# Performance work log

Hardware: AMD Instinct MI355X
Metric: run time of the kernel (lower is better)

## Reference

```python
import jax, jax.numpy as jnp
import numpy as np
from jax import lax

K = 16
EPS = 1e-5


def setup_inputs() -> dict:
    key = jax.random.key(0)
    k1, k2, k3 = jax.random.split(key, 3)
    x = jax.random.normal(k1, (8, 4096, 64), jnp.float32)
    pos = jax.random.normal(k2, (8, 4096, 3), jnp.float32)
    # nn.Linear(64,128), xavier_uniform weight, zero bias
    limit = float(np.sqrt(6.0 / (64 + 128)))
    W = jax.random.uniform(k3, (128, 64), jnp.float32, -limit, limit)
    b = jnp.zeros((128,), jnp.float32)
    gamma = jnp.ones((128,), jnp.float32)   # BN weight
    beta = jnp.zeros((128,), jnp.float32)   # BN bias
    return {"x": x, "pos": pos, "W": W, "b": b, "gamma": gamma, "beta": beta,
            "n_sampling": 1024}


def _fps(pos3, n_sampling):
    """Farthest point sampling starting at index 0. pos3: [bz,N,3] -> [bz,S] int32."""
    bz, N, _ = pos3.shape

    def step(carry, _):
        min_d, last = carry                                   # [bz,N], [bz]
        lastp = jnp.take_along_axis(pos3, last[:, None, None], axis=1)  # [bz,1,3]
        d = jnp.sum((pos3 - lastp) ** 2, axis=-1)             # [bz,N]
        min_d = jnp.minimum(min_d, d)
        nxt = jnp.argmax(min_d, axis=1).astype(jnp.int32)
        return (min_d, nxt), last

    init = (jnp.full((bz, N), 1e10, pos3.dtype), jnp.zeros((bz,), jnp.int32))
    _, idx = lax.scan(step, init, None, length=n_sampling)    # [S,bz]
    return idx.T                                              # [bz,S]


def _knn_idx(pos3, fps_idx, k):
    """k nearest neighbors (by squared L2) of sampled points among all N points."""
    spos = jnp.take_along_axis(pos3, fps_idx[..., None], axis=1)        # [bz,S,3]
    # ||a-b||^2 = |a|^2 + |b|^2 - 2 a.b, avoids [bz,S,N,3] intermediate
    d = (jnp.sum(spos ** 2, -1)[:, :, None]
         + jnp.sum(pos3 ** 2, -1)[:, None, :]
         - 2.0 * jnp.einsum('bsd,bnd->bsn', spos, pos3))               # [bz,S,N]
    _, idx = lax.top_k(-d, k)                                           # [bz,S,k]
    return idx


def reference(x, pos, W, b, gamma, beta, n_sampling):
    pos3 = pos[..., :3]
    fps_idx = _fps(pos3, n_sampling)                          # [bz,S]
    knn_idx = _knn_idx(pos3, fps_idx, K)                      # [bz,S,K]

    # Linear -> BatchNorm1d (training-mode batch stats, biased var) -> ReLU
    h = jnp.einsum('bnf,of->bno', x, W) + b                   # [bz,N,128]
    mean = h.mean(axis=(0, 1))
    var = h.var(axis=(0, 1))
    h = (h - mean) / jnp.sqrt(var + EPS) * gamma + beta
    h = jax.nn.relu(h)

    # gather k-NN features and max-pool (same math as expand+repeat+gather+max)
    gathered = jax.vmap(lambda hb, ib: hb[ib])(h, knn_idx)    # [bz,S,K,128]
    sampled_knn_x = gathered.max(axis=2)                      # [bz,S,128]

    sampled_pos = jnp.take_along_axis(pos, fps_idx[..., None], axis=1)  # [bz,S,3]
    return sampled_knn_x, sampled_pos
```

## Files before the change

### kernel.cpp

```cpp
#include <hip/hip_runtime.h>
#include <stdint.h>

typedef unsigned long long ull;
typedef float f32x2 __attribute__((ext_vector_type(2)));

#define NBATCH 8
#define NPTS   4096
#define NS     1024
#define NK     16
#define NF     64
#define NO     128

#define FT  256
#define PPT 16

static __device__ __forceinline__ ull umax64(ull a, ull b) { return a > b ? a : b; }
static __device__ __forceinline__ ull umin64(ull a, ull b) { return a < b ? a : b; }

static __device__ __forceinline__ float dist2(const float* plds, int i, float sx,
                                              float sy, float sz) {
  const float dx = plds[i * 3 + 0] - sx;
  const float dy = plds[i * 3 + 1] - sy;
  const float dz = plds[i * 3 + 2] - sz;
  return fmaf(dz, dz, fmaf(dy, dy, dx * dx));
}

static __device__ __forceinline__ ull dpp_min_u64(ull v) {
#define STEP(ctrl)                                                            \
  {                                                                           \
    const unsigned lo = (unsigned)v;                                          \
    const unsigned hi = (unsigned)(v >> 32);                                  \
    const unsigned olo = (unsigned)__builtin_amdgcn_update_dpp(               \
        (int)lo, (int)lo, ctrl, 0xf, 0xf, false);                             \
    const unsigned ohi = (unsigned)__builtin_amdgcn_update_dpp(               \
        (int)hi, (int)hi, ctrl, 0xf, 0xf, false);                             \
    const ull o = ((ull)ohi << 32) | olo;                                     \
    v = o < v ? o : v;                                                        \
  }
  STEP(0x111)
  STEP(0x112)
  STEP(0x114)
  STEP(0x118)
  STEP(0x142)
  STEP(0x143)
#undef STEP
  return v;
}

__global__ __launch_bounds__(256) void fps_stats_kernel(
    const float* __restrict__ pos, const float* __restrict__ x,
    const float* __restrict__ W, const float* __restrict__ bias,
    int* __restrict__ fps_idx, float* __restrict__ out_pos,
    float* __restrict__ partial) {
#pragma clang fp contract(off)
  const int t = threadIdx.x;
  __shared__ float plds[NPTS * 3];
  __shared__ __align__(16) ull wslot[2][4];
  __shared__ int widx_lds[NS];

  if (blockIdx.x >= 8) {
    const int blk = blockIdx.x - 8;
    const int c = t & 127;
    const int h = t >> 7;
    float* xl = plds;

    const float4* Wv = (const float4*)(W + c * NF);
    float4 w[16];
#pragma unroll
    for (int q = 0; q < 16; ++q) w[q] = Wv[q];
    const float bb = bias[c];

    const float4* src = (const float4*)(x + (size_t)blk * 128 * NF);
    float4* dst = (float4*)xl;
    for (int i = t; i < 128 * NF / 4; i += 256) dst[i] = src[i];
    __syncthreads();

    float s = 0.f, s2 = 0.f;
    for (int r = h * 64; r < h * 64 + 64; ++r) {
      const float4* xr = (const float4*)(xl + r * NF);
      float hh = bb;
#pragma unroll
      for (int q = 0; q < 16; ++q) {
        const float4 xv = xr[q];
        hh = fmaf(xv.x, w[q].x, hh);
        hh = fmaf(xv.y, w[q].y, hh);
        hh = fmaf(xv.z, w[q].z, hh);
        hh = fmaf(xv.w, w[q].w, hh);
      }
      s += hh;
      s2 = fmaf(hh, hh, s2);
    }
    partial[(blk * 2 + h) * 256 + c] = s;
    partial[(blk * 2 + h) * 256 + 128 + c] = s2;
    return;
  }

  const int b = blockIdx.x;
  const float* p = pos + (size_t)b * NPTS * 3;
  {
    const float4* src = (const float4*)p;
    float4* dst = (float4*)plds;
    for (int i = t; i < NPTS * 3 / 4; i += FT) dst[i] = src[i];
  }
  if (t == 0) widx_lds[0] = 0;
  __syncthreads();

  f32x2 px2[PPT / 2], py2[PPT / 2], pz2[PPT / 2], md2[PPT / 2];
#pragma unroll
  for (int jp = 0; jp < PPT / 2; ++jp) {
    const int i0 = t + FT * (2 * jp);
    const int i1 = i0 + FT;
    px2[jp] = (f32x2){plds[3 * i0 + 0], plds[3 * i1 + 0]};
    py2[jp] = (f32x2){plds[3 * i0 + 1], plds[3 * i1 + 1]};
    pz2[jp] = (f32x2){plds[3 * i0 + 2], plds[3 * i1 + 2]};
    md2[jp] = (f32x2){1e10f, 1e10f};
  }

  float lx = plds[0], ly = plds[1], lz = plds[2];

  for (int s = 1; s < NS; ++s) {
    const f32x2 lxv = (f32x2){lx, lx};
    const f32x2 lyv = (f32x2){ly, ly};
    const f32x2 lzv = (f32x2){lz, lz};
    f32x2 acc = (f32x2){0.f, 0.f};
#pragma unroll
    for (int jp = 0; jp < PPT / 2; ++jp) {
      const f32x2 dx = px2[jp] - lxv;
      const f32x2 dy = py2[jp] - lyv;
      const f32x2 dz = pz2[jp] - lzv;
      const f32x2 xx = dx * dx;
      const f32x2 yy = dy * dy;
      const f32x2 zz = dz * dz;
      const f32x2 sxy = xx + yy;
      const f32x2 d = sxy + zz;
      md2[jp] = __builtin_elementwise_min(md2[jp], d);
      acc = __builtin_elementwise_max(acc, md2[jp]);
    }
    float best = fmaxf(acc.x, acc.y);
    int lidx = 0;
#pragma unroll
    for (int jp = 0; jp < PPT / 2; ++jp) {
      if (md2[jp].x == best) lidx = t + FT * (2 * jp);
      if (md2[jp].y == best) lidx = t + FT * (2 * jp) + FT;
    }
#define CARRY_STEP(ctrl)                                                     \
    {                                                                        \
      const float bo = __int_as_float(__builtin_amdgcn_update_dpp(           \
          0, __float_as_int(best), ctrl, 0xf, 0xf, true));                   \
      const int io =                                                         \
          __builtin_amdgcn_update_dpp(0, lidx, ctrl, 0xf, 0xf, true);        \
      if (bo > best) {                                                       \
        best = bo;                                                           \
        lidx = io;                                                           \
      }                                                                      \
    }
    CARRY_STEP(0x111)
    CARRY_STEP(0x112)
    CARRY_STEP(0x114)
    CARRY_STEP(0x118)
    CARRY_STEP(0x142)
    CARRY_STEP(0x143)
#undef CARRY_STEP
    if ((t & 63) == 63)
      wslot[s & 1][t >> 6] = ((ull)__float_as_uint(best) << 32) | (unsigned)lidx;
    __syncthreads();
    const ull* wk = wslot[s & 1];
    const ull kk = umax64(umax64(wk[0], wk[1]), umax64(wk[2], wk[3]));
    const int widx = (int)(kk & 0xFFFFFFFFu);
    lx = plds[3 * widx + 0];
    ly = plds[3 * widx + 1];
    lz = plds[3 * widx + 2];
    if (t == 0) widx_lds[s] = widx;
  }

  __syncthreads();
  for (int i = t; i < NS; i += FT) {
    const int wi = widx_lds[i];
    fps_idx[b * NS + i] = wi;
    out_pos[((size_t)b * NS + i) * 3 + 0] = plds[3 * wi + 0];
    out_pos[((size_t)b * NS + i) * 3 + 1] = plds[3 * wi + 1];
    out_pos[((size_t)b * NS + i) * 3 + 2] = plds[3 * wi + 2];
  }
}

__global__ __launch_bounds__(1024) void stats_reduce_kernel(
    const float* __restrict__ partial, const float* __restrict__ gamma,
    const float* __restrict__ beta, float* __restrict__ ab) {
  const int t = threadIdx.x;
  const int c = t & 127;
  const int q = t >> 7;
  __shared__ double sred[1024], s2red[1024];
  double s = 0.0, s2 = 0.0;
#pragma unroll 4
  for (int r = q * 64; r < q * 64 + 64; ++r) {
    s += (double)partial[r * 256 + c];
    s2 += (double)partial[r * 256 + 128 + c];
  }
  sred[t] = s;
  s2red[t] = s2;
  __syncthreads();
  if (t < 128) {
    s = 0.0;
    s2 = 0.0;
#pragma unroll
    for (int qq = 0; qq < 8; ++qq) {
      s += sred[qq * 128 + t];
      s2 += s2red[qq * 128 + t];
    }
    const double n = 32768.0;
    const double mean = s / n;
    const double var = s2 / n - mean * mean;
    const float inv = (float)(1.0 / sqrt(var + 1e-5));
    const float scale = gamma[t] * inv;
    const float shift = beta[t] - (float)mean * scale;
    ab[t] = scale;
    ab[128 + t] = shift;
  }
}

__global__ __launch_bounds__(256) void knn_kernel(const float* __restrict__ pos,
                                                  const int* __restrict__ fps_idx,
                                                  int* __restrict__ knn_idx) {
  __shared__ float plds[NPTS * 3];
  const int b = blockIdx.y;
  const int t = threadIdx.x;
  const int s0 = blockIdx.x * 16;

  {
    const float4* src = (const float4*)(pos + (size_t)b * NPTS * 3);
    float4* dst = (float4*)plds;
    for (int i = t; i < NPTS * 3 / 4; i += 256) dst[i] = src[i];
  }
  __syncthreads();

  const int samp = t >> 4;
  const int chunk = t & 15;
  const int sidx = fps_idx[b * NS + s0 + samp];
  const float sx = plds[sidx * 3 + 0];
  const float sy = plds[sidx * 3 + 1];
  const float sz = plds[sidx * 3 + 2];

  ull k16[16];
#pragma unroll
  for (int k = 0; k < 16; ++k) k16[k] = 0xFFFFFFFF00000000ull | (unsigned)k;
  ull worst = 0xFFFFFFFF0000000Full;
  for (int j = 0; j < 256; ++j) {
    const int i = j * 16 + chunk;
    const float d = dist2(plds, i, sx, sy, sz);
    const ull key = ((ull)__float_as_uint(d) << 32) | (unsigned)i;
    if (key < worst) {
#pragma unroll
      for (int k = 0; k < 16; ++k) k16[k] = (k16[k] == worst) ? key : k16[k];
      ull w01 = umax64(k16[0], k16[1]);
      ull w2 = umax64(umax64(k16[2], k16[3]), umax64(k16[4], k16[5]));
      ull w3 = umax64(umax64(k16[6], k16[7]), umax64(k16[8], k16[9]));
      ull w4 = umax64(umax64(k16[10], k16[11]), umax64(k16[12], k16[13]));
      ull w5 = umax64(k16[14], k16[15]);
      worst = umax64(umax64(w01, w2), umax64(w3, umax64(w4, w5)));
    }
  }
  __syncthreads();
  ull* kbuf = (ull*)plds;
  {
    ull* dst = kbuf + samp * 256 + chunk * 16;
#pragma unroll
    for (int k = 0; k < 16; ++k) dst[k] = k16[k];
  }
  __syncthreads();

  const int wave = t >> 6;
  const int lane = t & 63;
  for (int si = 0; si < 4; ++si) {
    const int s = wave * 4 + si;
    const ull* src = kbuf + s * 256 + lane * 4;
    ull a0 = src[0], a1 = src[1], a2 = src[2], a3 = src[3];
    int kwin = 0;
#pragma unroll
    for (int k = 0; k < 16; ++k) {
      const ull mv = umin64(umin64(a0, a1), umin64(a2, a3));
      const ull wmin = dpp_min_u64(mv);
      const ull win = __shfl(wmin, 63, 64);
      if (lane == k) kwin = (int)(win & 0xFFFFFFFFu);
      a0 = (a0 == win) ? ~0ull : a0;
      a1 = (a1 == win) ? ~0ull : a1;
      a2 = (a2 == win) ? ~0ull : a2;
      a3 = (a3 == win) ? ~0ull : a3;
    }
    if (lane < 16)
      knn_idx[((size_t)b * NS + s0 + s) * NK + lane] = kwin;
  }
}

__global__ __launch_bounds__(256) void gather_kernel(
    const float* __restrict__ x, const float* __restrict__ W,
    const float* __restrict__ bias, const float* __restrict__ ab,
    const int* __restrict__ knn_idx, float* __restrict__ out) {
  __shared__ float xtile[64 * NF];
  const int b = blockIdx.y;
  const int t = threadIdx.x;
  const int s0 = blockIdx.x * 16;
  const int c2 = t & 63;
  const int g = t >> 6;

  float4 w0[16], w1[16];
  {
    const float4* Wv0 = (const float4*)(W + c2 * NF);
    const float4* Wv1 = (const float4*)(W + (c2 + 64) * NF);
#pragma unroll
    for (int q = 0; q < 16; ++q) {
      w0[q] = Wv0[q];
      w1[q] = Wv1[q];
    }
  }
  const float bb0 = bias[c2], bb1 = bias[c2 + 64];
  const float scale0 = ab[c2], scale1 = ab[c2 + 64];
  const float shift0 = ab[128 + c2], shift1 = ab[128 + c2 + 64];
  const float* xb = x + (size_t)b * NPTS * NF;

  for (int pass = 0; pass < 4; ++pass) {
    {
      const int r = t & 63;
      const int q0 = (t >> 6) * 4;
      const int idx =
          knn_idx[((size_t)b * NS + s0 + pass * 4 + (r >> 4)) * NK + (r & 15)];
      const float4* srow = (const float4*)(xb + (size_t)idx * NF);
      float4* drow = (float4*)(xtile + r * NF);
#pragma unroll
      for (int q = q0; q < q0 + 4; ++q) drow[q] = srow[q];
    }
    __syncthreads();

    float m0 = 0.0f, m1 = 0.0f;
#pragma unroll
    for (int k = 0; k < NK; ++k) {
      const float4* xr = (const float4*)(xtile + (g * 16 + k) * NF);
      float h0 = bb0, h1 = bb1;
#pragma unroll
      for (int q = 0; q < 16; ++q) {
        const float4 xv = xr[q];
        h0 = fmaf(xv.x, w0[q].x, h0);
        h0 = fmaf(xv.y, w0[q].y, h0);
        h0 = fmaf(xv.z, w0[q].z, h0);
        h0 = fmaf(xv.w, w0[q].w, h0);
        h1 = fmaf(xv.x, w1[q].x, h1);
        h1 = fmaf(xv.y, w1[q].y, h1);
        h1 = fmaf(xv.z, w1[q].z, h1);
        h1 = fmaf(xv.w, w1[q].w, h1);
      }
      h0 = fmaf(h0, scale0, shift0);
      h1 = fmaf(h1, scale1, shift1);
      h0 = h0 > 0.f ? h0 : 0.f;
      h1 = h1 > 0.f ? h1 : 0.f;
      m0 = m0 > h0 ? m0 : h0;
      m1 = m1 > h1 ? m1 : h1;
    }
    float* o = out + ((size_t)b * NS + s0 + pass * 4 + g) * NO;
    o[c2] = m0;
    o[c2 + 64] = m1;
    __syncthreads();
  }
}

extern "C" void kernel_launch(void* const* d_in, const int* in_sizes, int n_in,
                              void* d_out, int out_size, void* d_ws, size_t ws_size,
                              hipStream_t stream) {
  const float* x     = (const float*)d_in[0];
  const float* pos   = (const float*)d_in[1];
  const float* W     = (const float*)d_in[2];
  const float* bias  = (const float*)d_in[3];
  const float* gamma = (const float*)d_in[4];
  const float* beta  = (const float*)d_in[5];

  float* out_knn = (float*)d_out;
  float* out_pos = out_knn + (size_t)NBATCH * NS * NO;

  char* ws = (char*)d_ws;
  int* fps_idx   = (int*)(ws);
  float* partial = (float*)(ws + (32 << 10));
  int* knn_idx   = (int*)partial;
  float* ab      = (float*)(ws + (544 << 10));

  fps_stats_kernel<<<8 + 256, 256, 0, stream>>>(pos, x, W, bias, fps_idx,
                                                out_pos, partial);
  stats_reduce_kernel<<<1, 1024, 0, stream>>>(partial, gamma, beta, ab);
  knn_kernel<<<dim3(64, NBATCH), 256, 0, stream>>>(pos, fps_idx, knn_idx);
  gather_kernel<<<dim3(64, NBATCH), 256, 0, stream>>>(x, W, bias, ab, knn_idx,
                                                      out_knn);
}
```

Baseline: 910.3 us.

## Pack two FPS batches per 512-thread block sharing one barrier

Farthest-point sampling now runs two batch elements per workgroup of 512 threads, each half using its own LDS copy of positions and its own winner slots. Both halves pass the same per-iteration __syncthreads. Stats blocks are widened to 512 threads with an in-LDS pairwise reduction so the partial layout stays the same. This halves the number of FPS blocks and couples two independent serial chains at each barrier, which may add sync latency. The gain depends on how FPS blocks were placed across CUs before.

New measurement: 1.162 ms. 1.28x slower.

```diff
diff --git a/kernel.cpp b/kernel.cpp
--- a/kernel.cpp
+++ b/kernel.cpp
@@ -11,7 +11,6 @@
 #define NF     64
 #define NO     128
 
-#define FT  256
 #define PPT 16
 
 static __device__ __forceinline__ ull umax64(ull a, ull b) { return a > b ? a : b; }
@@ -47,22 +46,24 @@
   return v;
 }
 
-__global__ __launch_bounds__(256) void fps_stats_kernel(
+__global__ __launch_bounds__(512, 1) void fps_stats_kernel(
     const float* __restrict__ pos, const float* __restrict__ x,
     const float* __restrict__ W, const float* __restrict__ bias,
     int* __restrict__ fps_idx, float* __restrict__ out_pos,
     float* __restrict__ partial) {
 #pragma clang fp contract(off)
   const int t = threadIdx.x;
-  __shared__ float plds[NPTS * 3];
-  __shared__ __align__(16) ull wslot[2][4];
-  __shared__ int widx_lds[NS];
-
-  if (blockIdx.x >= 8) {
-    const int blk = blockIdx.x - 8;
+  __shared__ float plds[2][NPTS * 3];
+  __shared__ __align__(16) ull wslot[2][2][4];
+  __shared__ int widx_lds[2][NS];
+
+  if (blockIdx.x >= 4) {
+    const int blk = blockIdx.x - 4;
     const int c = t & 127;
     const int h = t >> 7;
-    float* xl = plds;
+    float* xl = plds[0];
+    float* sred = plds[1];
+    float* s2red = plds[1] + 512;
 
     const float4* Wv = (const float4*)(W + c * NF);
     float4 w[16];
@@ -72,11 +73,11 @@
 
     const float4* src = (const float4*)(x + (size_t)blk * 128 * NF);
     float4* dst = (float4*)xl;
-    for (int i = t; i < 128 * NF / 4; i += 256) dst[i] = src[i];
+    for (int i = t; i < 128 * NF / 4; i += 512) dst[i] = src[i];
     __syncthreads();
 
     float s = 0.f, s2 = 0.f;
-    for (int r = h * 64; r < h * 64 + 64; ++r) {
+    for (int r = h * 32; r < h * 32 + 32; ++r) {
       const float4* xr = (const float4*)(xl + r * NF);
       float hh = bb;
 #pragma unroll
@@ -90,33 +91,43 @@
       s += hh;
       s2 = fmaf(hh, hh, s2);
     }
-    partial[(blk * 2 + h) * 256 + c] = s;
-    partial[(blk * 2 + h) * 256 + 128 + c] = s2;
+    sred[t] = s;
+    s2red[t] = s2;
+    __syncthreads();
+    if (h < 2) {
+      s += sred[t + 256];
+      s2 += s2red[t + 256];
+      partial[(blk * 2 + h) * 256 + c] = s;
+      partial[(blk * 2 + h) * 256 + 128 + c] = s2;
+    }
     return;
   }
 
-  const int b = blockIdx.x;
-  const float* p = pos + (size_t)b * NPTS * 3;
+  const int grp = t >> 8;
+  const int tl = t & 255;
+  const int b = blockIdx.x * 2 + grp;
+  float* P = plds[grp];
+
   {
-    const float4* src = (const float4*)p;
-    float4* dst = (float4*)plds;
-    for (int i = t; i < NPTS * 3 / 4; i += FT) dst[i] = src[i];
-  }
-  if (t == 0) widx_lds[0] = 0;
+    const float4* src = (const float4*)(pos + (size_t)b * NPTS * 3);
+    float4* dst = (float4*)P;
+    for (int i = tl; i < NPTS * 3 / 4; i += 256) dst[i] = src[i];
+  }
+  if (tl == 0) widx_lds[grp][0] = 0;
   __syncthreads();
 
   f32x2 px2[PPT / 2], py2[PPT / 2], pz2[PPT / 2], md2[PPT / 2];
 #pragma unroll
   for (int jp = 0; jp < PPT / 2; ++jp) {
-    const int i0 = t + FT * (2 * jp);
-    const int i1 = i0 + FT;
-    px2[jp] = (f32x2){plds[3 * i0 + 0], plds[3 * i1 + 0]};
-    py2[jp] = (f32x2){plds[3 * i0 + 1], plds[3 * i1 + 1]};
-    pz2[jp] = (f32x2){plds[3 * i0 + 2], plds[3 * i1 + 2]};
+    const int i0 = tl + 256 * (2 * jp);
+    const int i1 = i0 + 256;
+    px2[jp] = (f32x2){P[3 * i0 + 0], P[3 * i1 + 0]};
+    py2[jp] = (f32x2){P[3 * i0 + 1], P[3 * i1 + 1]};
+    pz2[jp] = (f32x2){P[3 * i0 + 2], P[3 * i1 + 2]};
     md2[jp] = (f32x2){1e10f, 1e10f};
   }
 
-  float lx = plds[0], ly = plds[1], lz = plds[2];
+  float lx = P[0], ly = P[1], lz = P[2];
 
   for (int s = 1; s < NS; ++s) {
     const f32x2 lxv = (f32x2){lx, lx};
@@ -140,8 +151,8 @@
     int lidx = 0;
 #pragma unroll
     for (int jp = 0; jp < PPT / 2; ++jp) {
-      if (md2[jp].x == best) lidx = t + FT * (2 * jp);
-      if (md2[jp].y == best) lidx = t + FT * (2 * jp) + FT;
+      if (md2[jp].x == best) lidx = tl + 256 * (2 * jp);
+      if (md2[jp].y == best) lidx = tl + 256 * (2 * jp) + 256;
     }
 #define CARRY_STEP(ctrl)                                                     \
     {                                                                        \
@@ -161,25 +172,26 @@
     CARRY_STEP(0x142)
     CARRY_STEP(0x143)
 #undef CARRY_STEP
-    if ((t & 63) == 63)
-      wslot[s & 1][t >> 6] = ((ull)__float_as_uint(best) << 32) | (unsigned)lidx;
+    if ((tl & 63) == 63)
+      wslot[grp][s & 1][tl >> 6] =
+          ((ull)__float_as_uint(best) << 32) | (unsigned)lidx;
     __syncthreads();
-    const ull* wk = wslot[s & 1];
+    const ull* wk = wslot[grp][s & 1];
     const ull kk = umax64(umax64(wk[0], wk[1]), umax64(wk[2], wk[3]));
     const int widx = (int)(kk & 0xFFFFFFFFu);
-    lx = plds[3 * widx + 0];
-    ly = plds[3 * widx + 1];
-    lz = plds[3 * widx + 2];
-    if (t == 0) widx_lds[s] = widx;
-  }
-
-  __syncthreads();
-  for (int i = t; i < NS; i += FT) {
-    const int wi = widx_lds[i];
+    lx = P[3 * widx + 0];
+    ly = P[3 * widx + 1];
+    lz = P[3 * widx + 2];
+    if (tl == 0) widx_lds[grp][s] = widx;
+  }
+
+  __syncthreads();
+  for (int i = tl; i < NS; i += 256) {
+    const int wi = widx_lds[grp][i];
     fps_idx[b * NS + i] = wi;
-    out_pos[((size_t)b * NS + i) * 3 + 0] = plds[3 * wi + 0];
-    out_pos[((size_t)b * NS + i) * 3 + 1] = plds[3 * wi + 1];
-    out_pos[((size_t)b * NS + i) * 3 + 2] = plds[3 * wi + 2];
+    out_pos[((size_t)b * NS + i) * 3 + 0] = P[3 * wi + 0];
+    out_pos[((size_t)b * NS + i) * 3 + 1] = P[3 * wi + 1];
+    out_pos[((size_t)b * NS + i) * 3 + 2] = P[3 * wi + 2];
   }
 }
 
@@ -380,7 +392,7 @@
   int* knn_idx   = (int*)partial;
   float* ab      = (float*)(ws + (544 << 10));
 
-  fps_stats_kernel<<<8 + 256, 256, 0, stream>>>(pos, x, W, bias, fps_idx,
+  fps_stats_kernel<<<4 + 256, 512, 0, stream>>>(pos, x, W, bias, fps_idx,
                                                 out_pos, partial);
   stats_reduce_kernel<<<1, 1024, 0, stream>>>(partial, gamma, beta, ab);
   knn_kernel<<<dim3(64, NBATCH), 256, 0, stream>>>(pos, fps_idx, knn_idx);
```
